# Kernel optimization log

Hardware: AMD Instinct MI355X
Metric: run time of the kernel (lower is better)

## Reference

```python
import jax, jax.numpy as jnp
import numpy as np

N = 30000      # nodes
E = 240000     # edges (before self-loops)
D = 128        # vec_dim
L = 6          # GAT layers
NEG_SLOPE = 0.2
EPS = 1e-5


def setup_inputs() -> dict:
    key = jax.random.key(0)
    ks = jax.random.split(key, 20)
    s = 1.0 / np.sqrt(D)
    inp = {
        "x": jax.random.randint(ks[0], (N,), 0, 120),
        "edge_index": jax.random.randint(ks[1], (2, E), 0, N),
        "emb": jax.random.normal(ks[2], (120, D), jnp.float32) * 0.05,
        # stacked GATv2Conv params for 6 layers (heads=1)
        "Wl": jax.random.normal(ks[3], (L, D, D), jnp.float32) * s,
        "bl": jnp.zeros((L, D), jnp.float32),
        "Wr": jax.random.normal(ks[4], (L, D, D), jnp.float32) * s,
        "br": jnp.zeros((L, D), jnp.float32),
        "att": jax.random.normal(ks[5], (L, D), jnp.float32) * s,
        "conv_bias": jnp.zeros((L, D), jnp.float32),
        # PyG LayerNorm (applied after layers 0..4)
        "ln_g": jnp.ones((L - 1, D), jnp.float32),
        "ln_b": jnp.zeros((L - 1, D), jnp.float32),
        # outer Linear + BatchNorm1d
        "lin_W": jax.random.normal(ks[6], (D, D), jnp.float32) * s,
        "lin_b": jnp.zeros((D,), jnp.float32),
        "bn_g": jnp.ones((D,), jnp.float32),
        "bn_b": jnp.zeros((D,), jnp.float32),
    }
    return inp


def _segment_softmax(score, seg, num_segments):
    # numerically stable softmax over variable-degree neighborhoods
    m = jax.ops.segment_max(score, seg, num_segments=num_segments)
    ex = jnp.exp(score - m[seg])
    denom = jax.ops.segment_sum(ex, seg, num_segments=num_segments)
    return ex / denom[seg]


def _gat_forward(h, src, dst, Wl, bl, Wr, br, att, conv_bias, ln_g, ln_b):
    xg = h
    for i in range(L):
        xl = xg @ Wl[i] + bl[i]          # [N, D] source transform
        xr = xg @ Wr[i] + br[i]          # [N, D] target transform
        # GATv2 attention: a^T LeakyReLU(x_l[j] + x_r[i]) per edge j->i
        e = jax.nn.leaky_relu(xl[src] + xr[dst], NEG_SLOPE)   # [E2, D]
        score = e @ att[i]                                     # [E2]
        alpha = _segment_softmax(score, dst, N)                # [E2]
        msg = alpha[:, None] * xl[src]                         # [E2, D]
        xg = jax.ops.segment_sum(msg, dst, num_segments=N) + conv_bias[i]
        if i < L - 1:
            # PyG LayerNorm(mode='graph'): global mean/std, per-channel affine
            mu = xg.mean()
            var = ((xg - mu) ** 2).mean()
            xg = (xg - mu) / jnp.sqrt(var + EPS) * ln_g[i] + ln_b[i]
            xg = jax.nn.relu(xg)
            # dropout(0.1) is identity in eval mode
    return xg


def reference(x, edge_index, emb, Wl, bl, Wr, br, att, conv_bias,
              ln_g, ln_b, lin_W, lin_b, bn_g, bn_b):
    h = emb[x]                                      # [N, D]
    # PyG GATv2Conv default add_self_loops=True
    loops = jnp.arange(N, dtype=edge_index.dtype)
    src = jnp.concatenate([edge_index[0], loops])   # [E2]
    dst = jnp.concatenate([edge_index[1], loops])   # [E2]
    xg = _gat_forward(h, src, dst, Wl, bl, Wr, br, att, conv_bias, ln_g, ln_b)
    out = (h + xg) @ lin_W + lin_b                  # [N, D]
    # BatchNorm1d (batch-statistics / train-mode math)
    mu = out.mean(axis=0)
    var = out.var(axis=0)
    out = (out - mu) / jnp.sqrt(var + EPS) * bn_g + bn_b
    return out
```

## Files before the change

kernel.cpp:

```cpp
#include <hip/hip_runtime.h>
#include <math.h>

#define N_NODES 30000
#define N_EDGES 240000
#define E2 (N_EDGES + N_NODES)
#define D 128
#define LAYERS 6
#define NEG_SLOPE 0.2f
#define LN_EPS 1e-5f

typedef unsigned short u16;
typedef unsigned int u32;
using bfrag = __attribute__((ext_vector_type(8))) short;
using f32x4 = __attribute__((ext_vector_type(4))) float;

__device__ inline u16 f2bf(float f) {
    u32 u = __float_as_uint(f);
    u32 r = u + 0x7fffu + ((u >> 16) & 1u);
    return (u16)(r >> 16);
}
__device__ inline u32 pack2(float a, float b) { return (u32)f2bf(a) | ((u32)f2bf(b) << 16); }
__device__ inline float bflo(u32 u) { return __uint_as_float(u << 16); }
__device__ inline float bfhi(u32 u) { return __uint_as_float(u & 0xffff0000u); }
__device__ inline u32 bfadd2(u32 a, u32 b) {
    return pack2(bflo(a) + bflo(b), bfhi(a) + bfhi(b));
}

__device__ inline float red16_dpp(float x) {
    x += __int_as_float(__builtin_amdgcn_update_dpp(0, __float_as_int(x), 0xB1, 0xF, 0xF, true));
    x += __int_as_float(__builtin_amdgcn_update_dpp(0, __float_as_int(x), 0x4E, 0xF, 0xF, true));
    x += __int_as_float(__builtin_amdgcn_update_dpp(0, __float_as_int(x), 0x141, 0xF, 0xF, true));
    x += __int_as_float(__builtin_amdgcn_update_dpp(0, __float_as_int(x), 0x140, 0xF, 0xF, true));
    return x;
}

__global__ __launch_bounds__(256) void wt_convert(const float* __restrict__ Wl,
        const float* __restrict__ Wr, const float* __restrict__ linW, u16* __restrict__ wt)
{
    __shared__ u16 tile[128 * 129];
    int b = blockIdx.x;
    const float* src = (b == 12) ? linW
                     : ((b & 1) ? Wr + (size_t)(b >> 1) * 16384 : Wl + (size_t)(b >> 1) * 16384);
    int t = threadIdx.x;
    #pragma unroll 4
    for (int i = 0; i < 64; i++) {
        int idx = t + 256 * i;
        int k = idx >> 7, n = idx & 127;
        tile[n * 129 + k] = f2bf(src[idx]);
    }
    __syncthreads();
    u16* dst = wt + (size_t)b * 16384;
    #pragma unroll 4
    for (int i = 0; i < 64; i++) {
        int idx = t + 256 * i;
        int n = idx >> 7, k = idx & 127;
        dst[idx] = tile[n * 129 + k];
    }
}

__global__ __launch_bounds__(256) void hist_kernel(const int* __restrict__ ei, int* __restrict__ cnt)
{
    int e = blockIdx.x * 256 + threadIdx.x;
    if (e >= E2) return;
    int d = (e < N_EDGES) ? ei[N_EDGES + e] : (e - N_EDGES);
    atomicAdd(&cnt[d], 1);
}

__global__ __launch_bounds__(1024) void scan1_kernel(const int* __restrict__ cnt,
        int* __restrict__ lscan, int* __restrict__ bsum)
{
    __shared__ int wtot[16];
    int t = threadIdx.x, lane = t & 63, w = t >> 6;
    int i = blockIdx.x * 1024 + t;
    int v = (i < N_NODES) ? cnt[i] : 0;
    int s = v;
    #pragma unroll
    for (int off = 1; off < 64; off <<= 1) {
        int u = __shfl_up(s, off);
        if (lane >= off) s += u;
    }
    if (lane == 63) wtot[w] = s;
    __syncthreads();
    if (t < 16) {
        int xv = wtot[t];
        #pragma unroll
        for (int off = 1; off < 16; off <<= 1) {
            int u = __shfl_up(xv, off);
            if (t >= off) xv += u;
        }
        wtot[t] = xv;
    }
    __syncthreads();
    int incl = ((w == 0) ? 0 : wtot[w - 1]) + s;
    if (i < N_NODES) lscan[i] = incl;
    if (t == 0) bsum[blockIdx.x] = wtot[15];
}

__global__ __launch_bounds__(1024) void scan3_kernel(const int* __restrict__ lscan,
        const int* __restrict__ bsum, const int* __restrict__ cnt,
        int* __restrict__ row_off, int* __restrict__ cursor)
{
    __shared__ int sboff;
    if (threadIdx.x < 64) {
        int v = (threadIdx.x < 30) ? bsum[threadIdx.x] : 0;
        int s = v;
        #pragma unroll
        for (int off = 1; off < 64; off <<= 1) {
            int u = __shfl_up(s, off);
            if ((int)threadIdx.x >= off) s += u;
        }
        if (threadIdx.x == blockIdx.x) sboff = s - v;
    }
    __syncthreads();
    int i = blockIdx.x * 1024 + threadIdx.x;
    if (i == 0) row_off[0] = 0;
    if (i < N_NODES) {
        int r = lscan[i] + sboff;
        row_off[i + 1] = r;
        cursor[i] = r - cnt[i];
    }
}

__global__ __launch_bounds__(256) void scatter_kernel(const int* __restrict__ ei,
        int* __restrict__ cursor, int* __restrict__ csr_src)
{
    int e = blockIdx.x * 256 + threadIdx.x;
    if (e >= E2) return;
    int s, d;
    if (e < N_EDGES) { s = ei[e]; d = ei[N_EDGES + e]; }
    else             { s = e - N_EDGES; d = s; }
    int pos = atomicAdd(&cursor[d], 1);
    csr_src[pos] = s;
}

template<bool LN, bool DUAL, bool OUTF, bool EMB>
__global__ __launch_bounds__(256, 2) void gemm_mfma(
    const u16* __restrict__ Abf, const u16* __restrict__ A2bf,
    const float* __restrict__ Aln, const float* __restrict__ lnacc,
    const float* __restrict__ lng, const float* __restrict__ lnb,
    const int* __restrict__ xidx, const float* __restrict__ emb, u16* __restrict__ h_out,
    const u16* __restrict__ Wt1, const float* __restrict__ b1,
    float* __restrict__ C1f, u16* __restrict__ C1h,
    const u16* __restrict__ Wt2, const float* __restrict__ b2, u16* __restrict__ C2h,
    float* __restrict__ bnacc, int M)
{
    __shared__ u16 As[128 * 136];
    __shared__ float sLN[2];
    int t = threadIdx.x;
    int m0 = blockIdx.x * 128;
    int lane = t & 63, w = t >> 6;
    int n16 = lane & 15, quad = lane >> 4;
    int c0 = w * 32;

    bfrag bW1[2][4], bW2[2][4];
    #pragma unroll
    for (int c = 0; c < 2; c++)
        #pragma unroll
        for (int ks = 0; ks < 4; ks++)
            bW1[c][ks] = *(const bfrag*)(Wt1 + (size_t)(c0 + c * 16 + n16) * 128 + ks * 32 + quad * 8);
    if (DUAL) {
        #pragma unroll
        for (int c = 0; c < 2; c++)
            #pragma unroll
            for (int ks = 0; ks < 4; ks++)
                bW2[c][ks] = *(const bfrag*)(Wt2 + (size_t)(c0 + c * 16 + n16) * 128 + ks * 32 + quad * 8);
    }

    if (LN) {
        if (w == 0) {
            float2 v = ((const float2*)lnacc)[lane];
            float s = v.x, ss = v.y;
            #pragma unroll
            for (int off = 32; off > 0; off >>= 1) {
                s += __shfl_xor(s, off); ss += __shfl_xor(ss, off);
            }
            if (lane == 0) {
                const float invM = 1.f / ((float)N_NODES * (float)D);
                float mu  = s * invM;
                float var = ss * invM - mu * mu;
                sLN[0] = mu;
                sLN[1] = rsqrtf(var + LN_EPS);
            }
        }
        __syncthreads();
        float mu = sLN[0], inv = sLN[1];
        #pragma unroll
        for (int i = 0; i < 16; i++) {
            int idx = t + 256 * i;
            int row = idx >> 5, c4 = idx & 31;
            int gr = m0 + row;
            float4 v = make_float4(0.f, 0.f, 0.f, 0.f);
            if (gr < M) v = ((const float4*)(Aln + (size_t)gr * D))[c4];
            float4 gv = ((const float4*)lng)[c4];
            float4 bv = ((const float4*)lnb)[c4];
            v.x = (v.x - mu) * inv * gv.x + bv.x; v.x = v.x > 0.f ? v.x : 0.f;
            v.y = (v.y - mu) * inv * gv.y + bv.y; v.y = v.y > 0.f ? v.y : 0.f;
            v.z = (v.z - mu) * inv * gv.z + bv.z; v.z = v.z > 0.f ? v.z : 0.f;
            v.w = (v.w - mu) * inv * gv.w + bv.w; v.w = v.w > 0.f ? v.w : 0.f;
            uint2 pk = make_uint2(pack2(v.x, v.y), pack2(v.z, v.w));
            *(uint2*)&As[row * 136 + c4 * 4] = pk;
        }
    } else if (EMB) {
        #pragma unroll
        for (int i = 0; i < 8; i++) {
            int idx = t + 256 * i;
            int row = idx >> 4, c16 = idx & 15;
            int gr = m0 + row;
            uint4 v = make_uint4(0u, 0u, 0u, 0u);
            if (gr < M) {
                const float* er = emb + (size_t)xidx[gr] * D + c16 * 8;
                float4 e0 = ((const float4*)er)[0];
                float4 e1 = ((const float4*)er)[1];
                v.x = pack2(e0.x, e0.y); v.y = pack2(e0.z, e0.w);
                v.z = pack2(e1.x, e1.y); v.w = pack2(e1.z, e1.w);
                ((uint4*)(h_out + (size_t)gr * 128))[c16] = v;
            }
            *(uint4*)&As[row * 136 + c16 * 8] = v;
        }
    } else {
        #pragma unroll
        for (int i = 0; i < 8; i++) {
            int idx = t + 256 * i;
            int row = idx >> 4, c16 = idx & 15;
            int gr = m0 + row;
            uint4 v = make_uint4(0u, 0u, 0u, 0u);
            if (gr < M) {
                v = ((const uint4*)(Abf + (size_t)gr * 128))[c16];
                if (A2bf) {
                    uint4 u = ((const uint4*)(A2bf + (size_t)gr * 128))[c16];
                    v.x = bfadd2(v.x, u.x); v.y = bfadd2(v.y, u.y);
                    v.z = bfadd2(v.z, u.z); v.w = bfadd2(v.w, u.w);
                }
            }
            *(uint4*)&As[row * 136 + c16 * 8] = v;
        }
    }
    __syncthreads();

    f32x4 zero = {0.f, 0.f, 0.f, 0.f};
    f32x4 acc1[8][2], acc2[8][2];
    #pragma unroll
    for (int r = 0; r < 8; r++)
        #pragma unroll
        for (int c = 0; c < 2; c++) { acc1[r][c] = zero; if (DUAL) acc2[r][c] = zero; }

    #pragma unroll
    for (int ks = 0; ks < 4; ks++) {
        bfrag a[8];
        #pragma unroll
        for (int r = 0; r < 8; r++)
            a[r] = *(const bfrag*)&As[(r * 16 + n16) * 136 + ks * 32 + quad * 8];
        #pragma unroll
        for (int r = 0; r < 8; r++)
            #pragma unroll
            for (int c = 0; c < 2; c++) {
                acc1[r][c] = __builtin_amdgcn_mfma_f32_16x16x32_bf16(a[r], bW1[c][ks], acc1[r][c], 0, 0, 0);
                if (DUAL)
                    acc2[r][c] = __builtin_amdgcn_mfma_f32_16x16x32_bf16(a[r], bW2[c][ks], acc2[r][c], 0, 0, 0);
            }
    }

    float bv1[2] = { b1[c0 + n16], b1[c0 + 16 + n16] };
    float bns[2] = {0.f, 0.f}, bnss[2] = {0.f, 0.f};
    #pragma unroll
    for (int r = 0; r < 8; r++)
        #pragma unroll
        for (int c = 0; c < 2; c++)
            #pragma unroll
            for (int reg = 0; reg < 4; reg++) {
                int grow = m0 + r * 16 + quad * 4 + reg;
                if (grow < M) {
                    float val = acc1[r][c][reg] + bv1[c];
                    int col = c0 + c * 16 + n16;
                    if (OUTF) {
                        C1f[(size_t)grow * 128 + col] = val;
                        bns[c] += val; bnss[c] += val * val;
                    } else {
                        C1h[(size_t)grow * 128 + col] = f2bf(val);
                    }
                }
            }
    if (OUTF) {
        #pragma unroll
        for (int c = 0; c < 2; c++) {
            #pragma unroll
            for (int msk = 16; msk <= 32; msk <<= 1) {
                bns[c]  += __shfl_xor(bns[c], msk);
                bnss[c] += __shfl_xor(bnss[c], msk);
            }
        }
        if (quad == 0) {
            float* base = bnacc + (size_t)(blockIdx.x & 15) * 256;
            #pragma unroll
            for (int c = 0; c < 2; c++) {
                int col = c0 + c * 16 + n16;
                atomicAdd(&base[col], bns[c]);
                atomicAdd(&base[128 + col], bnss[c]);
            }
        }
    }
    if (DUAL) {
        float bv2[2] = { b2[c0 + n16], b2[c0 + 16 + n16] };
        #pragma unroll
        for (int r = 0; r < 8; r++)
            #pragma unroll
            for (int c = 0; c < 2; c++)
                #pragma unroll
                for (int reg = 0; reg < 4; reg++) {
                    int grow = m0 + r * 16 + quad * 4 + reg;
                    if (grow < M)
                        C2h[(size_t)grow * 128 + c0 + c * 16 + n16] = f2bf(acc2[r][c][reg] + bv2[c]);
                }
    }
}

__global__ __launch_bounds__(256) void gat_agg(
    const u16* __restrict__ xl, const u16* __restrict__ xr,
    const int* __restrict__ row_off, const int* __restrict__ csr_src,
    const float* __restrict__ att, const float* __restrict__ conv_bias,
    float* __restrict__ xg, u16* __restrict__ xg_bf, float* __restrict__ lnacc)
{
    int wave = threadIdx.x >> 6, lane = threadIdx.x & 63;
    int node = blockIdx.x * 4 + wave;
    int g = lane >> 4, q = lane & 15;

    uint4 rr = *(const uint4*)(xr + (size_t)node * 128 + q * 8);
    float4 r0 = make_float4(bflo(rr.x), bfhi(rr.x), bflo(rr.y), bfhi(rr.y));
    float4 r1 = make_float4(bflo(rr.z), bfhi(rr.z), bflo(rr.w), bfhi(rr.w));
    float4 av0 = ((const float4*)att)[2 * q];
    float4 av1 = ((const float4*)att)[2 * q + 1];

    int s0 = row_off[node], s1 = row_off[node + 1];
    float denom = 0.f;
    float4 a0 = make_float4(0.f, 0.f, 0.f, 0.f), a1 = a0;

    #pragma unroll 4
    for (int s = s0 + g; s < s1; s += 4) {
        int src = csr_src[s];
        uint4 raw = *(const uint4*)(xl + (size_t)src * 128 + q * 8);
        float4 v0 = make_float4(bflo(raw.x), bfhi(raw.x), bflo(raw.y), bfhi(raw.y));
        float4 v1 = make_float4(bflo(raw.z), bfhi(raw.z), bflo(raw.w), bfhi(raw.w));
        float pr = 0.f, tt;
        tt = v0.x + r0.x; tt = tt > 0.f ? tt : NEG_SLOPE * tt; pr += av0.x * tt;
        tt = v0.y + r0.y; tt = tt > 0.f ? tt : NEG_SLOPE * tt; pr += av0.y * tt;
        tt = v0.z + r0.z; tt = tt > 0.f ? tt : NEG_SLOPE * tt; pr += av0.z * tt;
        tt = v0.w + r0.w; tt = tt > 0.f ? tt : NEG_SLOPE * tt; pr += av0.w * tt;
        tt = v1.x + r1.x; tt = tt > 0.f ? tt : NEG_SLOPE * tt; pr += av1.x * tt;
        tt = v1.y + r1.y; tt = tt > 0.f ? tt : NEG_SLOPE * tt; pr += av1.y * tt;
        tt = v1.z + r1.z; tt = tt > 0.f ? tt : NEG_SLOPE * tt; pr += av1.z * tt;
        tt = v1.w + r1.w; tt = tt > 0.f ? tt : NEG_SLOPE * tt; pr += av1.w * tt;
        pr = red16_dpp(pr);
        float wv = __expf(pr);
        denom += wv;
        a0.x += wv * v0.x; a0.y += wv * v0.y; a0.z += wv * v0.z; a0.w += wv * v0.w;
        a1.x += wv * v1.x; a1.y += wv * v1.y; a1.z += wv * v1.z; a1.w += wv * v1.w;
    }

    #pragma unroll
    for (int msk = 16; msk <= 32; msk <<= 1) {
        denom += __shfl_xor(denom, msk);
        a0.x += __shfl_xor(a0.x, msk); a0.y += __shfl_xor(a0.y, msk);
        a0.z += __shfl_xor(a0.z, msk); a0.w += __shfl_xor(a0.w, msk);
        a1.x += __shfl_xor(a1.x, msk); a1.y += __shfl_xor(a1.y, msk);
        a1.z += __shfl_xor(a1.z, msk); a1.w += __shfl_xor(a1.w, msk);
    }

    float4 cb0 = ((const float4*)conv_bias)[2 * q];
    float4 cb1 = ((const float4*)conv_bias)[2 * q + 1];
    float inv = 1.f / denom;
    float4 o0, o1;
    o0.x = a0.x * inv + cb0.x; o0.y = a0.y * inv + cb0.y;
    o0.z = a0.z * inv + cb0.z; o0.w = a0.w * inv + cb0.w;
    o1.x = a1.x * inv + cb1.x; o1.y = a1.y * inv + cb1.y;
    o1.z = a1.z * inv + cb1.z; o1.w = a1.w * inv + cb1.w;

    if (xg_bf) {
        if (g == 0) {
            uint4 pk = make_uint4(pack2(o0.x, o0.y), pack2(o0.z, o0.w),
                                  pack2(o1.x, o1.y), pack2(o1.z, o1.w));
            ((uint4*)(xg_bf + (size_t)node * 128))[q] = pk;
        }
    } else {
        if (g == 0) {
            ((float4*)(xg + (size_t)node * 128))[2 * q]     = o0;
            ((float4*)(xg + (size_t)node * 128))[2 * q + 1] = o1;
        }
        float s  = o0.x + o0.y + o0.z + o0.w + o1.x + o1.y + o1.z + o1.w;
        float ss = o0.x*o0.x + o0.y*o0.y + o0.z*o0.z + o0.w*o0.w
                 + o1.x*o1.x + o1.y*o1.y + o1.z*o1.z + o1.w*o1.w;
        s  = red16_dpp(s);
        ss = red16_dpp(ss);
        __shared__ float sred[8];
        if (lane == 0) { sred[wave] = s; sred[4 + wave] = ss; }
        __syncthreads();
        if (threadIdx.x == 0) {
            int slot = blockIdx.x & 63;
            atomicAdd(&lnacc[2 * slot],     sred[0] + sred[1] + sred[2] + sred[3]);
            atomicAdd(&lnacc[2 * slot + 1], sred[4] + sred[5] + sred[6] + sred[7]);
        }
    }
}

__global__ __launch_bounds__(256) void bn_apply(float* __restrict__ out, const float* __restrict__ acc,
        const float* __restrict__ g, const float* __restrict__ b)
{
    int idx = blockIdx.x * 256 + threadIdx.x;
    if (idx >= N_NODES * 32) return;
    int c4 = idx & 31;
    float4 s1 = make_float4(0.f, 0.f, 0.f, 0.f), s2 = s1;
    #pragma unroll
    for (int slot = 0; slot < 16; slot++) {
        float4 a = ((const float4*)(acc + slot * 256))[c4];
        float4 d = ((const float4*)(acc + slot * 256 + 128))[c4];
        s1.x += a.x; s1.y += a.y; s1.z += a.z; s1.w += a.w;
        s2.x += d.x; s2.y += d.y; s2.z += d.z; s2.w += d.w;
    }
    float4 gv = ((const float4*)g)[c4];
    float4 bv = ((const float4*)b)[c4];
    float4 v = ((float4*)out)[idx];
    const float invN = 1.f / (float)N_NODES;
    float mu, var, inv;
    mu = s1.x * invN; var = s2.x * invN - mu * mu; inv = rsqrtf(var + LN_EPS);
    v.x = (v.x - mu) * inv * gv.x + bv.x;
    mu = s1.y * invN; var = s2.y * invN - mu * mu; inv = rsqrtf(var + LN_EPS);
    v.y = (v.y - mu) * inv * gv.y + bv.y;
    mu = s1.z * invN; var = s2.z * invN - mu * mu; inv = rsqrtf(var + LN_EPS);
    v.z = (v.z - mu) * inv * gv.z + bv.z;
    mu = s1.w * invN; var = s2.w * invN - mu * mu; inv = rsqrtf(var + LN_EPS);
    v.w = (v.w - mu) * inv * gv.w + bv.w;
    ((float4*)out)[idx] = v;
}

extern "C" void kernel_launch(void* const* d_in, const int* in_sizes, int n_in,
                              void* d_out, int out_size, void* d_ws, size_t ws_size,
                              hipStream_t stream)
{
    const int*   x    = (const int*)d_in[0];
    const int*   ei   = (const int*)d_in[1];
    const float* emb  = (const float*)d_in[2];
    const float* Wl   = (const float*)d_in[3];
    const float* bl   = (const float*)d_in[4];
    const float* Wr   = (const float*)d_in[5];
    const float* br   = (const float*)d_in[6];
    const float* att  = (const float*)d_in[7];
    const float* cbias= (const float*)d_in[8];
    const float* lng  = (const float*)d_in[9];
    const float* lnb  = (const float*)d_in[10];
    const float* linW = (const float*)d_in[11];
    const float* linb = (const float*)d_in[12];
    const float* bng  = (const float*)d_in[13];
    const float* bnb  = (const float*)d_in[14];
    float* out = (float*)d_out;

    char* p = (char*)d_ws;
    float* xg    = (float*)p; p += (size_t)N_NODES * D * 4;
    u16*   xl_bf = (u16*)p;   p += (size_t)N_NODES * D * 2;
    u16*   xr_bf = (u16*)p;   p += (size_t)N_NODES * D * 2;
    u16*   xg_bf = (u16*)p;   p += (size_t)N_NODES * D * 2;
    u16*   h_bf  = (u16*)p;   p += (size_t)N_NODES * D * 2;
    u16*   wt    = (u16*)p;   p += (size_t)13 * 16384 * 2;
    int* cnt     = (int*)p; p += ((N_NODES * 4 + 255) / 256) * 256;
    int* lscan   = (int*)p; p += ((N_NODES * 4 + 255) / 256) * 256;
    int* row_off = (int*)p; p += (((N_NODES + 1) * 4 + 255) / 256) * 256;
    int* cursor  = (int*)p; p += ((N_NODES * 4 + 255) / 256) * 256;
    int* csr_src = (int*)p; p += ((E2 * 4 + 255) / 256) * 256;
    int* bsum    = (int*)p; p += 256;
    float* accs  = (float*)p; p += 20480;

    hipMemsetAsync(cnt, 0, N_NODES * 4, stream);
    hipMemsetAsync(accs, 0, (640 + 4096) * 4, stream);

    wt_convert<<<13, 256, 0, stream>>>(Wl, Wr, linW, wt);
    hist_kernel<<<(E2 + 255) / 256, 256, 0, stream>>>(ei, cnt);
    scan1_kernel<<<30, 1024, 0, stream>>>(cnt, lscan, bsum);
    scan3_kernel<<<30, 1024, 0, stream>>>(lscan, bsum, cnt, row_off, cursor);
    scatter_kernel<<<(E2 + 255) / 256, 256, 0, stream>>>(ei, cursor, csr_src);

    const int GEMM_GRID = (N_NODES + 127) / 128;
    for (int i = 0; i < LAYERS; i++) {
        if (i == 0) {
            gemm_mfma<false, true, false, true><<<GEMM_GRID, 256, 0, stream>>>(
                nullptr, nullptr, nullptr, nullptr, nullptr, nullptr,
                x, emb, h_bf,
                wt + (size_t)0 * 16384, bl + 0, nullptr, xl_bf,
                wt + (size_t)1 * 16384, br + 0, xr_bf, nullptr, N_NODES);
        } else {
            gemm_mfma<true, true, false, false><<<GEMM_GRID, 256, 0, stream>>>(
                nullptr, nullptr, xg, accs + (i - 1) * 128,
                lng + (size_t)(i - 1) * D, lnb + (size_t)(i - 1) * D,
                nullptr, nullptr, nullptr,
                wt + (size_t)(2 * i) * 16384, bl + i * D, nullptr, xl_bf,
                wt + (size_t)(2 * i + 1) * 16384, br + i * D, xr_bf, nullptr, N_NODES);
        }
        gat_agg<<<7500, 256, 0, stream>>>(xl_bf, xr_bf, row_off, csr_src,
            att + i * D, cbias + i * D, xg,
            (i == LAYERS - 1) ? xg_bf : nullptr,
            (i < LAYERS - 1) ? (accs + i * 128) : nullptr);
    }
    gemm_mfma<false, false, true, false><<<GEMM_GRID, 256, 0, stream>>>(
        xg_bf, h_bf, nullptr, nullptr, nullptr, nullptr,
        nullptr, nullptr, nullptr,
        wt + (size_t)12 * 16384, linb, out, nullptr,
        nullptr, nullptr, nullptr, accs + 640, N_NODES);
    bn_apply<<<3750, 256, 0, stream>>>(out, accs + 640, bng, bnb);
}
```

Measured before the change: 585.2 us.

## Split dual GEMM across grid y and shrink row tile to 32

The fused Wl/Wr GEMM used to compute both outputs in one 128-row block. It now uses 32-row blocks, and a second grid dimension selects which weight, bias and output each block handles. This gives many more blocks and fewer registers per thread, which should improve occupancy and load balance. In exchange, the A tile (including the LayerNorm or embedding preprocessing) is loaded and recomputed twice, and the weights are reloaded per smaller tile.

```diff
diff --git a/kernel.cpp b/kernel.cpp
--- a/kernel.cpp
+++ b/kernel.cpp
@@ -133,8 +133,8 @@
     csr_src[pos] = s;
 }
 
-template<bool LN, bool DUAL, bool OUTF, bool EMB>
-__global__ __launch_bounds__(256, 2) void gemm_mfma(
+template<bool LN, bool OUTF, bool EMB>
+__global__ __launch_bounds__(256) void gemm_mfma(
     const u16* __restrict__ Abf, const u16* __restrict__ A2bf,
     const float* __restrict__ Aln, const float* __restrict__ lnacc,
     const float* __restrict__ lng, const float* __restrict__ lnb,
@@ -144,27 +144,23 @@
     const u16* __restrict__ Wt2, const float* __restrict__ b2, u16* __restrict__ C2h,
     float* __restrict__ bnacc, int M)
 {
-    __shared__ u16 As[128 * 136];
+    __shared__ u16 As[32 * 136];
     __shared__ float sLN[2];
+    const u16*  Wt   = blockIdx.y ? Wt2 : Wt1;
+    const float* bias = blockIdx.y ? b2 : b1;
+    u16*        Ch   = blockIdx.y ? C2h : C1h;
     int t = threadIdx.x;
-    int m0 = blockIdx.x * 128;
+    int m0 = blockIdx.x * 32;
     int lane = t & 63, w = t >> 6;
     int n16 = lane & 15, quad = lane >> 4;
     int c0 = w * 32;
 
-    bfrag bW1[2][4], bW2[2][4];
+    bfrag bW[2][4];
     #pragma unroll
     for (int c = 0; c < 2; c++)
         #pragma unroll
         for (int ks = 0; ks < 4; ks++)
-            bW1[c][ks] = *(const bfrag*)(Wt1 + (size_t)(c0 + c * 16 + n16) * 128 + ks * 32 + quad * 8);
-    if (DUAL) {
-        #pragma unroll
-        for (int c = 0; c < 2; c++)
-            #pragma unroll
-            for (int ks = 0; ks < 4; ks++)
-                bW2[c][ks] = *(const bfrag*)(Wt2 + (size_t)(c0 + c * 16 + n16) * 128 + ks * 32 + quad * 8);
-    }
+            bW[c][ks] = *(const bfrag*)(Wt + (size_t)(c0 + c * 16 + n16) * 128 + ks * 32 + quad * 8);
 
     if (LN) {
         if (w == 0) {
@@ -185,7 +181,7 @@
         __syncthreads();
         float mu = sLN[0], inv = sLN[1];
         #pragma unroll
-        for (int i = 0; i < 16; i++) {
+        for (int i = 0; i < 4; i++) {
             int idx = t + 256 * i;
             int row = idx >> 5, c4 = idx & 31;
             int gr = m0 + row;
@@ -202,7 +198,7 @@
         }
     } else if (EMB) {
         #pragma unroll
-        for (int i = 0; i < 8; i++) {
+        for (int i = 0; i < 2; i++) {
             int idx = t + 256 * i;
             int row = idx >> 4, c16 = idx & 15;
             int gr = m0 + row;
@@ -213,13 +209,14 @@
                 float4 e1 = ((const float4*)er)[1];
                 v.x = pack2(e0.x, e0.y); v.y = pack2(e0.z, e0.w);
                 v.z = pack2(e1.x, e1.y); v.w = pack2(e1.z, e1.w);
-                ((uint4*)(h_out + (size_t)gr * 128))[c16] = v;
+                if (blockIdx.y == 0)
+                    ((uint4*)(h_out + (size_t)gr * 128))[c16] = v;
             }
             *(uint4*)&As[row * 136 + c16 * 8] = v;
         }
     } else {
         #pragma unroll
-        for (int i = 0; i < 8; i++) {
+        for (int i = 0; i < 2; i++) {
             int idx = t + 256 * i;
             int row = idx >> 4, c16 = idx & 15;
             int gr = m0 + row;
@@ -238,45 +235,37 @@
     __syncthreads();
 
     f32x4 zero = {0.f, 0.f, 0.f, 0.f};
-    f32x4 acc1[8][2], acc2[8][2];
-    #pragma unroll
-    for (int r = 0; r < 8; r++)
-        #pragma unroll
-        for (int c = 0; c < 2; c++) { acc1[r][c] = zero; if (DUAL) acc2[r][c] = zero; }
-
+    f32x4 acc[2][2] = {{zero, zero}, {zero, zero}};
     #pragma unroll
     for (int ks = 0; ks < 4; ks++) {
-        bfrag a[8];
-        #pragma unroll
-        for (int r = 0; r < 8; r++)
+        bfrag a[2];
+        #pragma unroll
+        for (int r = 0; r < 2; r++)
             a[r] = *(const bfrag*)&As[(r * 16 + n16) * 136 + ks * 32 + quad * 8];
         #pragma unroll
-        for (int r = 0; r < 8; r++)
+        for (int r = 0; r < 2; r++)
             #pragma unroll
-            for (int c = 0; c < 2; c++) {
-                acc1[r][c] = __builtin_amdgcn_mfma_f32_16x16x32_bf16(a[r], bW1[c][ks], acc1[r][c], 0, 0, 0);
-                if (DUAL)
-                    acc2[r][c] = __builtin_amdgcn_mfma_f32_16x16x32_bf16(a[r], bW2[c][ks], acc2[r][c], 0, 0, 0);
-            }
-    }
-
-    float bv1[2] = { b1[c0 + n16], b1[c0 + 16 + n16] };
+            for (int c = 0; c < 2; c++)
+                acc[r][c] = __builtin_amdgcn_mfma_f32_16x16x32_bf16(a[r], bW[c][ks], acc[r][c], 0, 0, 0);
+    }
+
+    float bv[2] = { bias[c0 + n16], bias[c0 + 16 + n16] };
     float bns[2] = {0.f, 0.f}, bnss[2] = {0.f, 0.f};
     #pragma unroll
-    for (int r = 0; r < 8; r++)
+    for (int r = 0; r < 2; r++)
         #pragma unroll
         for (int c = 0; c < 2; c++)
             #pragma unroll
             for (int reg = 0; reg < 4; reg++) {
                 int grow = m0 + r * 16 + quad * 4 + reg;
                 if (grow < M) {
-                    float val = acc1[r][c][reg] + bv1[c];
+                    float val = acc[r][c][reg] + bv[c];
                     int col = c0 + c * 16 + n16;
                     if (OUTF) {
                         C1f[(size_t)grow * 128 + col] = val;
                         bns[c] += val; bnss[c] += val * val;
                     } else {
-                        C1h[(size_t)grow * 128 + col] = f2bf(val);
+                        Ch[(size_t)grow * 128 + col] = f2bf(val);
                     }
                 }
             }
@@ -298,19 +287,6 @@
                 atomicAdd(&base[128 + col], bnss[c]);
             }
         }
-    }
-    if (DUAL) {
-        float bv2[2] = { b2[c0 + n16], b2[c0 + 16 + n16] };
-        #pragma unroll
-        for (int r = 0; r < 8; r++)
-            #pragma unroll
-            for (int c = 0; c < 2; c++)
-                #pragma unroll
-                for (int reg = 0; reg < 4; reg++) {
-                    int grow = m0 + r * 16 + quad * 4 + reg;
-                    if (grow < M)
-                        C2h[(size_t)grow * 128 + c0 + c * 16 + n16] = f2bf(acc2[r][c][reg] + bv2[c]);
-                }
     }
 }
 
@@ -476,16 +452,16 @@
     scan3_kernel<<<30, 1024, 0, stream>>>(lscan, bsum, cnt, row_off, cursor);
     scatter_kernel<<<(E2 + 255) / 256, 256, 0, stream>>>(ei, cursor, csr_src);
 
-    const int GEMM_GRID = (N_NODES + 127) / 128;
+    const int GX = (N_NODES + 31) / 32;
     for (int i = 0; i < LAYERS; i++) {
         if (i == 0) {
-            gemm_mfma<false, true, false, true><<<GEMM_GRID, 256, 0, stream>>>(
+            gemm_mfma<false, false, true><<<dim3(GX, 2), 256, 0, stream>>>(
                 nullptr, nullptr, nullptr, nullptr, nullptr, nullptr,
                 x, emb, h_bf,
                 wt + (size_t)0 * 16384, bl + 0, nullptr, xl_bf,
                 wt + (size_t)1 * 16384, br + 0, xr_bf, nullptr, N_NODES);
         } else {
-            gemm_mfma<true, true, false, false><<<GEMM_GRID, 256, 0, stream>>>(
+            gemm_mfma<true, false, false><<<dim3(GX, 2), 256, 0, stream>>>(
                 nullptr, nullptr, xg, accs + (i - 1) * 128,
                 lng + (size_t)(i - 1) * D, lnb + (size_t)(i - 1) * D,
                 nullptr, nullptr, nullptr,
@@ -497,7 +473,7 @@
             (i == LAYERS - 1) ? xg_bf : nullptr,
             (i < LAYERS - 1) ? (accs + i * 128) : nullptr);
     }
-    gemm_mfma<false, false, true, false><<<GEMM_GRID, 256, 0, stream>>>(
+    gemm_mfma<false, true, false><<<dim3(GX, 1), 256, 0, stream>>>(
         xg_bf, h_bf, nullptr, nullptr, nullptr, nullptr,
         nullptr, nullptr, nullptr,
         wt + (size_t)12 * 16384, linb, out, nullptr,
```

Result: faster. 536.1 us (-8.4%).
